# Kernel tuning notes

Measured on AMD Instinct MI355X. Metric: run time of the kernel, lower is better.

Reference implementation:

```python
import jax, jax.numpy as jnp
import numpy as np

DECAY = 0.99
EPS = 1e-05
B, K, D = 32768, 8192, 512


def setup_inputs() -> dict:
    key = jax.random.key(0)
    k1, k2, k3 = jax.random.split(key, 3)
    return {
        "z_e": jax.random.normal(k1, (B, D), dtype=jnp.float32),
        "codebook": jax.random.normal(k2, (K, D), dtype=jnp.float32),
        "ema_cluster_size": jnp.zeros((K,), dtype=jnp.float32),
        "ema_codebook": jax.random.normal(k3, (K, D), dtype=jnp.float32),
    }


def reference(z_e, codebook, ema_cluster_size, ema_codebook):
    # The original weights (z_e - cb) by w = clamp(2*sign(z_e)+1, max=1) which is
    # always +/-1, so ||w*(z-c)|| == ||z-c||. Use the squared-distance GEMM
    # expansion instead of materializing the (B, K, D) broadcast tensor.
    # squared distances (B, K); argmin is invariant to the monotone sqrt.
    z_sq = jnp.sum(z_e * z_e, axis=-1, keepdims=True)          # (B, 1)
    c_sq = jnp.sum(codebook * codebook, axis=-1)               # (K,)
    d2 = z_sq - 2.0 * (z_e @ codebook.T) + c_sq[None, :]       # (B, K)
    indices = jnp.argmin(d2, axis=-1)                           # (B,)
    z_q = codebook[indices]                                     # (B, D)

    # Training-mode EMA update (the one-hot.T @ z_e scatter-matmul, done as
    # segment sums, which is the efficient equivalent of the one-hot matmul).
    counts = jax.ops.segment_sum(jnp.ones((z_e.shape[0],), z_e.dtype), indices,
                                 num_segments=K)                # (K,)
    embed_sum = jax.ops.segment_sum(z_e, indices, num_segments=K)  # (K, D)
    new_cluster_size = DECAY * ema_cluster_size + (1.0 - DECAY) * counts
    new_ema_codebook = DECAY * ema_codebook + (1.0 - DECAY) * embed_sum
    new_codebook = new_ema_codebook / (new_cluster_size + EPS)[:, None]

    return z_q, indices, new_codebook, new_cluster_size, new_ema_codebook
```

## Files before the change

### kernel.cpp

```cpp
#include <hip/hip_runtime.h>
#include <cfloat>

#define B_SZ 32768
#define K_SZ 8192
#define D_SZ 512

static constexpr float DECAY = 0.99f;
static constexpr float OMD   = 1.0f - 0.99f;
static constexpr float EPS   = 1e-5f;

typedef __attribute__((ext_vector_type(8))) __bf16 bf16x8;
typedef __attribute__((ext_vector_type(4))) float  f32x4;

#define ZQF_ZBF    0
#define ZQF_CBBF   8388608
#define ZQF_PART   10485760
#define NCF_CSQ    0
#define NCF_ZSQ    8192
#define NCF_MAXC   40960
#define NCF_WLCNT  40961
#define NCF_GCNT   40964
#define NCF_CUR    41092
#define NCF_SLOTS  41220
#define NCF_WL     106756
#define WL_CAP     4000000

__global__ __launch_bounds__(256)
void rowsq_kernel(const float* __restrict__ src, float* __restrict__ dst) {
    const int wave = threadIdx.x >> 6;
    const int lane = threadIdx.x & 63;
    const int r = blockIdx.x * 4 + wave;
    const float* row = src + (size_t)r * D_SZ;
    float s = 0.f;
#pragma unroll
    for (int i = 0; i < 2; ++i) {
        float4 v = *reinterpret_cast<const float4*>(row + i * 256 + lane * 4);
        s += v.x * v.x + v.y * v.y + v.z * v.z + v.w * v.w;
    }
#pragma unroll
    for (int off = 32; off >= 1; off >>= 1) s += __shfl_xor(s, off);
    if (lane == 0) dst[r] = s;
}

__global__ __launch_bounds__(256)
void maxinit_kernel(const float* __restrict__ c_sq, float* __restrict__ maxcsq,
                    int* __restrict__ wl_count, int* __restrict__ gcnt) {
    __shared__ float sm[4];
    float m = 0.f;
    for (int i = threadIdx.x; i < K_SZ; i += 256) m = fmaxf(m, c_sq[i]);
#pragma unroll
    for (int off = 32; off >= 1; off >>= 1) m = fmaxf(m, __shfl_xor(m, off));
    if ((threadIdx.x & 63) == 0) sm[threadIdx.x >> 6] = m;
    __syncthreads();
    if (threadIdx.x < 128) gcnt[threadIdx.x] = 0;
    if (threadIdx.x == 0) {
        maxcsq[0] = fmaxf(fmaxf(sm[0], sm[1]), fmaxf(sm[2], sm[3]));
        wl_count[0] = 0;
    }
}

__device__ __forceinline__ unsigned f2bf(float f) {
    unsigned u = __float_as_uint(f);
    return (u + 0x7FFFu + ((u >> 16) & 1u)) >> 16;
}
__global__ __launch_bounds__(256)
void cvt_kernel(const float* __restrict__ src, unsigned short* __restrict__ dst) {
    const size_t i = ((size_t)blockIdx.x * 256 + threadIdx.x) * 8;
    float4 a = *reinterpret_cast<const float4*>(src + i);
    float4 b = *reinterpret_cast<const float4*>(src + i + 4);
    uint4 o;
    o.x = f2bf(a.x) | (f2bf(a.y) << 16);
    o.y = f2bf(a.z) | (f2bf(a.w) << 16);
    o.z = f2bf(b.x) | (f2bf(b.y) << 16);
    o.w = f2bf(b.z) | (f2bf(b.w) << 16);
    *reinterpret_cast<uint4*>(dst + i) = o;
}

__global__ __launch_bounds__(256)
void init_ema_kernel(const float* __restrict__ ema_cb,
                     const float* __restrict__ ema_cs,
                     float* __restrict__ o_nemcb,
                     float* __restrict__ o_ncs) {
    const size_t i = (size_t)blockIdx.x * 256 + threadIdx.x;
    float4 e = *reinterpret_cast<const float4*>(ema_cb + i * 4);
    e.x *= DECAY; e.y *= DECAY; e.z *= DECAY; e.w *= DECAY;
    *reinterpret_cast<float4*>(o_nemcb + i * 4) = e;
    if (i < K_SZ) o_ncs[i] = DECAY * ema_cs[i];
}

__global__ __launch_bounds__(256, 3)
void gemm_approx(const unsigned short* __restrict__ zbf,
                 const unsigned short* __restrict__ cbbf,
                 const float* __restrict__ c_sq,
                 float* __restrict__ partials)
{
    __shared__ char lds[20480];

    const int tid  = threadIdx.x;
    const int lane = tid & 63;
    const int wid  = tid >> 6;
    const int wr   = wid >> 1;
    const int wc   = wid & 1;
    const int rb   = blockIdx.x >> 6;
    const int cb   = blockIdx.x & 63;
    const int b0   = rb * 128;
    const int k0   = cb * 128;

    f32x4 acc[4][4];
#pragma unroll
    for (int m = 0; m < 4; ++m)
#pragma unroll
        for (int n = 0; n < 4; ++n) acc[m][n] = 0.f;

    const int srow  = tid >> 1;
    const int shalf = tid & 1;
    const unsigned short* gz = zbf  + (size_t)(b0 + srow) * 512 + shalf * 16;
    const unsigned short* gc = cbbf + (size_t)(k0 + srow) * 512 + shalf * 16;
    char* wA = lds +         srow * 80 + shalf * 32;
    char* wB = lds + 10240 + srow * 80 + shalf * 32;
    const int fro = (lane & 15) * 80 + (lane >> 4) * 16;

#pragma unroll 1
    for (int kk = 0; kk < 16; ++kk) {
        uint4 vz0 = *reinterpret_cast<const uint4*>(gz + kk * 32);
        uint4 vz1 = *reinterpret_cast<const uint4*>(gz + kk * 32 + 8);
        uint4 vc0 = *reinterpret_cast<const uint4*>(gc + kk * 32);
        uint4 vc1 = *reinterpret_cast<const uint4*>(gc + kk * 32 + 8);
        __syncthreads();
        *reinterpret_cast<uint4*>(wA)      = vz0;
        *reinterpret_cast<uint4*>(wA + 16) = vz1;
        *reinterpret_cast<uint4*>(wB)      = vc0;
        *reinterpret_cast<uint4*>(wB + 16) = vc1;
        __syncthreads();

        bf16x8 af[4], bfr[4];
#pragma unroll
        for (int m = 0; m < 4; ++m)
            af[m] = *reinterpret_cast<const bf16x8*>(
                lds + (wr * 64 + m * 16) * 80 + fro);
#pragma unroll
        for (int n = 0; n < 4; ++n)
            bfr[n] = *reinterpret_cast<const bf16x8*>(
                lds + 10240 + (wc * 64 + n * 16) * 80 + fro);
#pragma unroll
        for (int m = 0; m < 4; ++m)
#pragma unroll
            for (int n = 0; n < 4; ++n)
                acc[m][n] = __builtin_amdgcn_mfma_f32_16x16x32_bf16(
                    af[m], bfr[n], acc[m][n], 0, 0, 0);
    }

    float csq[4];
#pragma unroll
    for (int n = 0; n < 4; ++n)
        csq[n] = c_sq[k0 + wc * 64 + n * 16 + (lane & 15)];

    float mn[16];
#pragma unroll
    for (int m = 0; m < 4; ++m) {
#pragma unroll
        for (int r = 0; r < 4; ++r) {
            float v = fmaf(-2.f, acc[m][0][r], csq[0]);
            v = fminf(v, fmaf(-2.f, acc[m][1][r], csq[1]));
            v = fminf(v, fmaf(-2.f, acc[m][2][r], csq[2]));
            v = fminf(v, fmaf(-2.f, acc[m][3][r], csq[3]));
#pragma unroll
            for (int off = 1; off <= 8; off <<= 1)
                v = fminf(v, __shfl_xor(v, off));
            mn[m * 4 + r] = v;
        }
    }
    if ((lane & 15) == 0) {
#pragma unroll
        for (int m = 0; m < 4; ++m)
#pragma unroll
            for (int r = 0; r < 4; ++r)
                partials[(size_t)(b0 + wr * 64 + m * 16 + (lane >> 4) * 4 + r) * 128
                         + cb * 2 + wc] = mn[m * 4 + r];
    }
}

__global__ __launch_bounds__(256)
void reduce2_kernel(const float* __restrict__ partials,
                    const float* __restrict__ z_sq,
                    const float* __restrict__ maxcsq,
                    int* __restrict__ gcnt,
                    unsigned long long* __restrict__ slots)
{
    const int row  = blockIdx.x * 4 + (threadIdx.x >> 6);
    const int lane = threadIdx.x & 63;
    const float p0 = partials[(size_t)row * 128 + lane];
    const float p1 = partials[(size_t)row * 128 + 64 + lane];
    float m = fminf(p0, p1);
#pragma unroll
    for (int off = 1; off <= 32; off <<= 1) m = fminf(m, __shfl_xor(m, off));
    const float thr = 0.0225f * sqrtf(z_sq[row] * maxcsq[0]) + 0.3f;
    const float lim = m + thr;
    if (lane == 0) slots[row] = 0xFFFFFFFFFFFFFFFFull;
    if (p0 <= lim) atomicAdd(gcnt + lane, 1);
    if (p1 <= lim) atomicAdd(gcnt + 64 + lane, 1);
}

__global__ void scan_kernel(const int* __restrict__ gcnt,
                            int* __restrict__ cursor,
                            int* __restrict__ wl_count) {
    if (threadIdx.x == 0 && blockIdx.x == 0) {
        int run = 0;
        for (int g = 0; g < 128; ++g) { cursor[g] = run; run += gcnt[g]; }
        wl_count[0] = run;
    }
}

__global__ __launch_bounds__(256)
void place_kernel(const float* __restrict__ partials,
                  const float* __restrict__ z_sq,
                  const float* __restrict__ maxcsq,
                  int* __restrict__ cursor,
                  int* __restrict__ wl)
{
    const int row  = blockIdx.x * 4 + (threadIdx.x >> 6);
    const int lane = threadIdx.x & 63;
    const float p0 = partials[(size_t)row * 128 + lane];
    const float p1 = partials[(size_t)row * 128 + 64 + lane];
    float m = fminf(p0, p1);
#pragma unroll
    for (int off = 1; off <= 32; off <<= 1) m = fminf(m, __shfl_xor(m, off));
    const float thr = 0.0225f * sqrtf(z_sq[row] * maxcsq[0]) + 0.3f;
    const float lim = m + thr;
    if (p0 <= lim) {
        int pos = atomicAdd(cursor + lane, 1);
        if (pos < WL_CAP) wl[pos] = row * 128 + lane;
    }
    if (p1 <= lim) {
        int pos = atomicAdd(cursor + 64 + lane, 1);
        if (pos < WL_CAP) wl[pos] = row * 128 + 64 + lane;
    }
}

__global__ __launch_bounds__(256, 2)
void rescore_kernel(const float* __restrict__ z_e,
                    const float* __restrict__ codebook,
                    const float* __restrict__ c_sq,
                    const float* __restrict__ z_sq,
                    const int* __restrict__ wl_count,
                    const int* __restrict__ wl,
                    unsigned long long* __restrict__ slots)
{
    __shared__ float zl[4][512];
    __shared__ float cl[4][32][65];
    const int tid = threadIdx.x, wid = tid >> 6, lane = tid & 63;
    const int nwaves = gridDim.x * 4;
    const int wgid = blockIdx.x * 4 + wid;
    const int total = wl_count[0];

    for (int i = wgid; i < total; i += nwaves) {
        const int e = wl[i];
        const int row = e >> 7;
        const int g = e & 127;
        const int kb = g * 64;
        {
            float4 a = *reinterpret_cast<const float4*>(z_e + (size_t)row * 512 + lane * 8);
            float4 b = *reinterpret_cast<const float4*>(z_e + (size_t)row * 512 + lane * 8 + 4);
            *reinterpret_cast<float4*>(&zl[wid][lane * 8])     = a;
            *reinterpret_cast<float4*>(&zl[wid][lane * 8 + 4]) = b;
        }
        float acc = 0.f;
        for (int dc = 0; dc < 16; ++dc) {
#pragma unroll
            for (int rg = 0; rg < 8; ++rg) {
                const int rr  = rg * 8 + (lane >> 3);
                const int dd0 = (lane & 7) * 4;
                float4 v = *reinterpret_cast<const float4*>(
                    codebook + (size_t)(kb + rr) * 512 + dc * 32 + dd0);
                cl[wid][dd0 + 0][rr] = v.x;
                cl[wid][dd0 + 1][rr] = v.y;
                cl[wid][dd0 + 2][rr] = v.z;
                cl[wid][dd0 + 3][rr] = v.w;
            }
#pragma unroll 8
            for (int dd = 0; dd < 32; ++dd)
                acc = fmaf(zl[wid][dc * 32 + dd], cl[wid][dd][lane], acc);
        }
        float v = fmaf(-2.f, acc, z_sq[row]) + c_sq[kb + lane];
        int idx = kb + lane;
#pragma unroll
        for (int off = 1; off <= 32; off <<= 1) {
            float v2 = __shfl_xor(v, off);
            int   i2 = __shfl_xor(idx, off);
            if (v2 < v || (v2 == v && i2 < idx)) { v = v2; idx = i2; }
        }
        if (lane == 0)
            atomicMin(slots + row,
                      ((unsigned long long)__float_as_uint(v) << 32) | (unsigned)idx);
    }
}

__global__ __launch_bounds__(256)
void scatter_kernel(const float* __restrict__ z_e,
                    const float* __restrict__ codebook,
                    const unsigned long long* __restrict__ slots,
                    float* __restrict__ z_q,
                    float* __restrict__ o_idx,
                    float* __restrict__ o_ncs,
                    float* __restrict__ o_nemcb)
{
    const int wave = threadIdx.x >> 6;
    const int lane = threadIdx.x & 63;
    const int b = blockIdx.x * 4 + wave;
    const int idx = (int)(unsigned)(slots[b] & 0xFFFFFFFFull);
#pragma unroll
    for (int i = 0; i < 2; ++i) {
        int d = i * 256 + lane * 4;
        float4 cq = *reinterpret_cast<const float4*>(
            codebook + (size_t)idx * D_SZ + d);
        *reinterpret_cast<float4*>(z_q + (size_t)b * D_SZ + d) = cq;
        float4 zv = *reinterpret_cast<const float4*>(
            z_e + (size_t)b * D_SZ + d);
        atomicAdd(o_nemcb + (size_t)idx * D_SZ + d + 0, OMD * zv.x);
        atomicAdd(o_nemcb + (size_t)idx * D_SZ + d + 1, OMD * zv.y);
        atomicAdd(o_nemcb + (size_t)idx * D_SZ + d + 2, OMD * zv.z);
        atomicAdd(o_nemcb + (size_t)idx * D_SZ + d + 3, OMD * zv.w);
    }
    if (lane == 0) {
        atomicAdd(o_ncs + idx, OMD);
        o_idx[b] = (float)idx;
    }
}

__global__ __launch_bounds__(256)
void finalize_kernel(const float* __restrict__ o_nemcb,
                     const float* __restrict__ o_ncs,
                     float* __restrict__ o_ncb)
{
    const size_t i = (size_t)blockIdx.x * 256 + threadIdx.x;
    const int k = (int)(i >> 7);
    float4 nem = *reinterpret_cast<const float4*>(o_nemcb + i * 4);
    float den = o_ncs[k] + EPS;
    float4 ncb;
    ncb.x = nem.x / den; ncb.y = nem.y / den;
    ncb.z = nem.z / den; ncb.w = nem.w / den;
    *reinterpret_cast<float4*>(o_ncb + i * 4) = ncb;
}

extern "C" void kernel_launch(void* const* d_in, const int* in_sizes, int n_in,
                              void* d_out, int out_size, void* d_ws, size_t ws_size,
                              hipStream_t stream) {
    const float* z_e      = (const float*)d_in[0];
    const float* codebook = (const float*)d_in[1];
    const float* ema_cs   = (const float*)d_in[2];
    const float* ema_cb   = (const float*)d_in[3];

    float* out = (float*)d_out;
    float* o_zq    = out;
    float* o_idx   = out + (size_t)B_SZ * D_SZ;
    float* o_ncb   = o_idx + B_SZ;
    float* o_ncs   = o_ncb + (size_t)K_SZ * D_SZ;
    float* o_nemcb = o_ncs + K_SZ;

    unsigned short* w_zbf  = (unsigned short*)(o_zq + ZQF_ZBF);
    unsigned short* w_cbbf = (unsigned short*)(o_zq + ZQF_CBBF);
    float*          w_part = o_zq + ZQF_PART;
    float*          w_csq  = o_ncb + NCF_CSQ;
    float*          w_zsq  = o_ncb + NCF_ZSQ;
    float*          w_maxc = o_ncb + NCF_MAXC;
    int*            w_cnt  = (int*)(o_ncb + NCF_WLCNT);
    int*            w_gcnt = (int*)(o_ncb + NCF_GCNT);
    int*            w_cur  = (int*)(o_ncb + NCF_CUR);
    unsigned long long* w_slots = (unsigned long long*)(o_ncb + NCF_SLOTS);
    int*            w_wl   = (int*)(o_ncb + NCF_WL);

    rowsq_kernel<<<K_SZ / 4, 256, 0, stream>>>(codebook, w_csq);
    rowsq_kernel<<<B_SZ / 4, 256, 0, stream>>>(z_e, w_zsq);
    maxinit_kernel<<<1, 256, 0, stream>>>(w_csq, w_maxc, w_cnt, w_gcnt);
    cvt_kernel<<<(int)((size_t)B_SZ * D_SZ / 2048), 256, 0, stream>>>(z_e, w_zbf);
    cvt_kernel<<<(int)((size_t)K_SZ * D_SZ / 2048), 256, 0, stream>>>(codebook, w_cbbf);
    init_ema_kernel<<<K_SZ * D_SZ / 4 / 256, 256, 0, stream>>>(
        ema_cb, ema_cs, o_nemcb, o_ncs);
    gemm_approx<<<(B_SZ / 128) * (K_SZ / 128), 256, 0, stream>>>(
        w_zbf, w_cbbf, w_csq, w_part);
    reduce2_kernel<<<B_SZ / 4, 256, 0, stream>>>(
        w_part, w_zsq, w_maxc, w_gcnt, w_slots);
    scan_kernel<<<1, 64, 0, stream>>>(w_gcnt, w_cur, w_cnt);
    place_kernel<<<B_SZ / 4, 256, 0, stream>>>(
        w_part, w_zsq, w_maxc, w_cur, w_wl);
    rescore_kernel<<<1024, 256, 0, stream>>>(
        z_e, codebook, w_csq, w_zsq, w_cnt, w_wl, w_slots);
    scatter_kernel<<<B_SZ / 4, 256, 0, stream>>>(
        z_e, codebook, w_slots, o_zq, o_idx, o_ncs, o_nemcb);
    finalize_kernel<<<K_SZ * D_SZ / 4 / 256, 256, 0, stream>>>(
        o_nemcb, o_ncs, o_ncb);
}
```

Before: 1.736 ms.

## Pre-transpose codebook so rescore reads coalesced float4 columns without LDS staging

Adds a kernel that writes the fp32 codebook into a D-group-major layout (float4 per k, grouped by four dimensions) inside the z_q output scratch region, after the approximate GEMM has consumed the bf16 copy there. The rescore kernel then reads each lane's codebook column directly from global memory with coalesced float4 loads, dropping the per-wave LDS transpose tile and its bank-conflicting stores. The rescore grid is doubled to 2048 blocks now that LDS use is lower. The cost is an extra 16 MB transpose pass, and the scratch reuse depends on the bf16 z buffer no longer being needed at that point.

```diff
diff --git a/kernel.cpp b/kernel.cpp
--- a/kernel.cpp
+++ b/kernel.cpp
@@ -13,6 +13,7 @@
 typedef __attribute__((ext_vector_type(4))) float  f32x4;
 
 #define ZQF_ZBF    0
+#define ZQF_CBT    0
 #define ZQF_CBBF   8388608
 #define ZQF_PART   10485760
 #define NCF_CSQ    0
@@ -181,6 +182,22 @@
 }
 
 __global__ __launch_bounds__(256)
+void transpose_kernel(const float* __restrict__ codebook,
+                      float4* __restrict__ cbT4)
+{
+    const int kpart = blockIdx.x & 31;
+    const int dpart = blockIdx.x >> 5;
+    const int k = kpart * 256 + threadIdx.x;
+#pragma unroll
+    for (int i = 0; i < 8; ++i) {
+        const int dg = dpart * 8 + i;
+        float4 v = *reinterpret_cast<const float4*>(
+            codebook + (size_t)k * D_SZ + dg * 4);
+        cbT4[(size_t)dg * K_SZ + k] = v;
+    }
+}
+
+__global__ __launch_bounds__(256)
 void reduce2_kernel(const float* __restrict__ partials,
                     const float* __restrict__ z_sq,
                     const float* __restrict__ maxcsq,
@@ -239,7 +256,7 @@
 
 __global__ __launch_bounds__(256, 2)
 void rescore_kernel(const float* __restrict__ z_e,
-                    const float* __restrict__ codebook,
+                    const float4* __restrict__ cbT4,
                     const float* __restrict__ c_sq,
                     const float* __restrict__ z_sq,
                     const int* __restrict__ wl_count,
@@ -247,7 +264,6 @@
                     unsigned long long* __restrict__ slots)
 {
     __shared__ float zl[4][512];
-    __shared__ float cl[4][32][65];
     const int tid = threadIdx.x, wid = tid >> 6, lane = tid & 63;
     const int nwaves = gridDim.x * 4;
     const int wgid = blockIdx.x * 4 + wid;
@@ -256,30 +272,23 @@
     for (int i = wgid; i < total; i += nwaves) {
         const int e = wl[i];
         const int row = e >> 7;
-        const int g = e & 127;
-        const int kb = g * 64;
+        const int kb = (e & 127) * 64;
         {
             float4 a = *reinterpret_cast<const float4*>(z_e + (size_t)row * 512 + lane * 8);
             float4 b = *reinterpret_cast<const float4*>(z_e + (size_t)row * 512 + lane * 8 + 4);
             *reinterpret_cast<float4*>(&zl[wid][lane * 8])     = a;
             *reinterpret_cast<float4*>(&zl[wid][lane * 8 + 4]) = b;
         }
+        const float4* cp = cbT4 + kb + lane;
         float acc = 0.f;
-        for (int dc = 0; dc < 16; ++dc) {
-#pragma unroll
-            for (int rg = 0; rg < 8; ++rg) {
-                const int rr  = rg * 8 + (lane >> 3);
-                const int dd0 = (lane & 7) * 4;
-                float4 v = *reinterpret_cast<const float4*>(
-                    codebook + (size_t)(kb + rr) * 512 + dc * 32 + dd0);
-                cl[wid][dd0 + 0][rr] = v.x;
-                cl[wid][dd0 + 1][rr] = v.y;
-                cl[wid][dd0 + 2][rr] = v.z;
-                cl[wid][dd0 + 3][rr] = v.w;
-            }
 #pragma unroll 8
-            for (int dd = 0; dd < 32; ++dd)
-                acc = fmaf(zl[wid][dc * 32 + dd], cl[wid][dd][lane], acc);
+        for (int dg = 0; dg < 128; ++dg) {
+            const float4 cv = cp[(size_t)dg * K_SZ];
+            const float4 zv = *reinterpret_cast<const float4*>(&zl[wid][dg * 4]);
+            acc = fmaf(zv.x, cv.x, acc);
+            acc = fmaf(zv.y, cv.y, acc);
+            acc = fmaf(zv.z, cv.z, acc);
+            acc = fmaf(zv.w, cv.w, acc);
         }
         float v = fmaf(-2.f, acc, z_sq[row]) + c_sq[kb + lane];
         int idx = kb + lane;
@@ -359,6 +368,7 @@
 
     unsigned short* w_zbf  = (unsigned short*)(o_zq + ZQF_ZBF);
     unsigned short* w_cbbf = (unsigned short*)(o_zq + ZQF_CBBF);
+    float4*         w_cbt  = (float4*)(o_zq + ZQF_CBT);
     float*          w_part = o_zq + ZQF_PART;
     float*          w_csq  = o_ncb + NCF_CSQ;
     float*          w_zsq  = o_ncb + NCF_ZSQ;
@@ -378,13 +388,14 @@
         ema_cb, ema_cs, o_nemcb, o_ncs);
     gemm_approx<<<(B_SZ / 128) * (K_SZ / 128), 256, 0, stream>>>(
         w_zbf, w_cbbf, w_csq, w_part);
+    transpose_kernel<<<512, 256, 0, stream>>>(codebook, w_cbt);
     reduce2_kernel<<<B_SZ / 4, 256, 0, stream>>>(
         w_part, w_zsq, w_maxc, w_gcnt, w_slots);
     scan_kernel<<<1, 64, 0, stream>>>(w_gcnt, w_cur, w_cnt);
     place_kernel<<<B_SZ / 4, 256, 0, stream>>>(
         w_part, w_zsq, w_maxc, w_cur, w_wl);
-    rescore_kernel<<<1024, 256, 0, stream>>>(
-        z_e, codebook, w_csq, w_zsq, w_cnt, w_wl, w_slots);
+    rescore_kernel<<<2048, 256, 0, stream>>>(
+        z_e, w_cbt, w_csq, w_zsq, w_cnt, w_wl, w_slots);
     scatter_kernel<<<B_SZ / 4, 256, 0, stream>>>(
         z_e, codebook, w_slots, o_zq, o_idx, o_ncs, o_nemcb);
     finalize_kernel<<<K_SZ * D_SZ / 4 / 256, 256, 0, stream>>>(
```

New measurement: 1.495 ms. 13.9% less time.
